# Performance work log

Hardware: AMD Instinct MI355X
Metric: run time of the kernel (lower is better)

The kernel has to match this reference:

```python
import jax, jax.numpy as jnp
import numpy as np

N_NODES = 100000
N_EDGES = 3200000
D = 256
REPEAT = 2
FACTOR = 0.5


def setup_inputs() -> dict:
    key = jax.random.key(0)
    k1, k2, k3, k4, k5, k6 = jax.random.split(key, 6)
    x = jax.random.normal(k1, (N_NODES, D), dtype=jnp.float32)
    vals = jax.random.uniform(k2, (N_EDGES,), dtype=jnp.float32)
    # Xavier-ish scale for linear weights
    W0 = jax.random.normal(k3, (D, D), dtype=jnp.float32) / np.sqrt(D)
    W1 = jax.random.normal(k4, (D, D), dtype=jnp.float32) / np.sqrt(D)
    rows = jax.random.randint(k5, (N_EDGES,), 0, N_NODES, dtype=jnp.int32)
    cols = jax.random.randint(k6, (N_EDGES,), 0, N_NODES, dtype=jnp.int32)
    return {"x": x, "vals": vals, "W0": W0, "W1": W1, "rows": rows, "cols": cols}


def reference(x, vals, W0, W1, rows, cols):
    # support is sparse [N, N] in COO: support[rows[e], cols[e]] = vals[e]
    def spmm(h):
        # gather source-node features, scale by edge weight, scatter-add to dst
        return jax.ops.segment_sum(vals[:, None] * h[cols], rows,
                                   num_segments=N_NODES)

    h = x
    for W, act in ((W0, jax.nn.relu), (W1, lambda v: v)):
        # _propagate: repeated SpMM with scalar factor
        for _ in range(REPEAT):
            h = spmm(h) * FACTOR
        # linear (no bias) + activation
        h = act(h @ W)
    return h
```

## Files before the change

### kernel.cpp

```cpp
#include <hip/hip_runtime.h>
#include <hip/hip_bf16.h>
#include <hip/hip_fp16.h>

#define N_D 256
#define NBLK 832
#define CPB 104
#define RPG_MAX 12512

typedef __attribute__((ext_vector_type(8))) short bf16x8;
typedef __attribute__((ext_vector_type(4))) float f32x4;

__device__ __forceinline__ unsigned short f2bf(float f) {
  union { float f; unsigned u; } c; c.f = f;
  unsigned u = c.u;
  return (unsigned short)((u + 0x7fffu + ((u >> 16) & 1u)) >> 16);
}
__device__ __forceinline__ float asf(unsigned u) {
  union { unsigned u; float f; } c; c.u = u;
  return c.f;
}
__device__ __forceinline__ int grp_of(int r, unsigned gmagic) {
  int g = (int)(((unsigned long long)(unsigned)r * gmagic) >> 37);
  return min(g, 7);
}

template <bool AF32>
__device__ __forceinline__ void gemm_core(
    const void* __restrict__ H, const unsigned short* __restrict__ WT,
    unsigned short* __restrict__ C, int M, int bid) {
  const int wave = threadIdx.x >> 6;
  const int lane = threadIdx.x & 63;
  const int m = lane & 15;
  const int p = lane >> 4;
  const int row0 = bid * 128 + wave * 32;

  f32x4 acc0[16], acc1[16];
#pragma unroll
  for (int i = 0; i < 16; ++i) {
    acc0[i] = (f32x4){0.f, 0.f, 0.f, 0.f};
    acc1[i] = (f32x4){0.f, 0.f, 0.f, 0.f};
  }

  const int r0 = row0 + m;
  const int r1 = row0 + 16 + m;
  const bool ok0 = r0 < M, ok1 = r1 < M;

  for (int k0 = 0; k0 < N_D; k0 += 32) {
    bf16x8 a0 = {0,0,0,0,0,0,0,0}, a1 = {0,0,0,0,0,0,0,0};
    if (AF32) {
      if (ok0) {
        const float* ap = (const float*)H + (size_t)r0 * N_D + k0 + p * 8;
        const float4 f0 = *reinterpret_cast<const float4*>(ap);
        const float4 f1 = *reinterpret_cast<const float4*>(ap + 4);
        a0[0]=f2bf(f0.x); a0[1]=f2bf(f0.y); a0[2]=f2bf(f0.z); a0[3]=f2bf(f0.w);
        a0[4]=f2bf(f1.x); a0[5]=f2bf(f1.y); a0[6]=f2bf(f1.z); a0[7]=f2bf(f1.w);
      }
      if (ok1) {
        const float* ap = (const float*)H + (size_t)r1 * N_D + k0 + p * 8;
        const float4 f0 = *reinterpret_cast<const float4*>(ap);
        const float4 f1 = *reinterpret_cast<const float4*>(ap + 4);
        a1[0]=f2bf(f0.x); a1[1]=f2bf(f0.y); a1[2]=f2bf(f0.z); a1[3]=f2bf(f0.w);
        a1[4]=f2bf(f1.x); a1[5]=f2bf(f1.y); a1[6]=f2bf(f1.z); a1[7]=f2bf(f1.w);
      }
    } else {
      if (ok0) a0 = *reinterpret_cast<const bf16x8*>(
          (const unsigned short*)H + (size_t)r0 * N_D + k0 + p * 8);
      if (ok1) a1 = *reinterpret_cast<const bf16x8*>(
          (const unsigned short*)H + (size_t)r1 * N_D + k0 + p * 8);
    }
#pragma unroll
    for (int nt = 0; nt < 16; ++nt) {
      const bf16x8 b = *reinterpret_cast<const bf16x8*>(
          WT + (size_t)(nt * 16 + m) * N_D + k0 + p * 8);
      acc0[nt] = __builtin_amdgcn_mfma_f32_16x16x32_bf16(a0, b, acc0[nt], 0, 0, 0);
      acc1[nt] = __builtin_amdgcn_mfma_f32_16x16x32_bf16(a1, b, acc1[nt], 0, 0, 0);
    }
  }

#pragma unroll
  for (int nt = 0; nt < 16; ++nt) {
    const int col = nt * 16 + m;
#pragma unroll
    for (int rr = 0; rr < 4; ++rr) {
      const int ra = row0 + p * 4 + rr;
      const int rb = ra + 16;
      if (ra < M) C[(size_t)ra * N_D + col] = f2bf(acc0[nt][rr]);
      if (rb < M) C[(size_t)rb * N_D + col] = f2bf(acc1[nt][rr]);
    }
  }
}

__global__ __launch_bounds__(256) void gemm3_f32(
    const float* __restrict__ H, const unsigned short* __restrict__ WT,
    unsigned short* __restrict__ C, int M) {
  gemm_core<true>(H, WT, C, M, blockIdx.x);
}
__global__ __launch_bounds__(256) void gemm3_bf16(
    const unsigned short* __restrict__ H, const unsigned short* __restrict__ WT,
    unsigned short* __restrict__ C, int M) {
  gemm_core<false>(H, WT, C, M, blockIdx.x);
}

__global__ __launch_bounds__(256) void p0_kernel(
    const int* __restrict__ rows, int* __restrict__ cntT,
    int n_edges, unsigned gmagic,
    const float* __restrict__ W0, const float* __restrict__ W1,
    unsigned short* __restrict__ WT0, unsigned short* __restrict__ WT1) {
  if (blockIdx.x >= NBLK) {
    const int b = blockIdx.x - NBLK;
    const int w = b >> 8;
    const int k = b & 255;
    const int n = threadIdx.x;
    const float* W = w ? W1 : W0;
    unsigned short* WT = w ? WT1 : WT0;
    WT[(size_t)n * N_D + k] = f2bf(W[(size_t)k * N_D + n]);
    return;
  }
  __shared__ int l8[8];
  if (threadIdx.x < 8) l8[threadIdx.x] = 0;
  __syncthreads();
  for (int e = blockIdx.x * 256 + threadIdx.x; e < n_edges; e += NBLK * 256) {
    atomicAdd(&l8[grp_of(rows[e], gmagic)], 1);
  }
  __syncthreads();
  if (threadIdx.x < 8) cntT[threadIdx.x * NBLK + blockIdx.x] = l8[threadIdx.x];
}

__global__ __launch_bounds__(256) void scan_one(
    const int* __restrict__ in, int* __restrict__ out, int n) {
  __shared__ int swsum[4];
  __shared__ int carry_sh;
  const int tid = threadIdx.x;
  const int lane = tid & 63;
  const int wid = tid >> 6;
  if (tid == 0) carry_sh = 0;
  __syncthreads();
  for (int base = 0; base < n; base += 1024) {
    const int i0 = base + tid * 4;
    int4 v = make_int4(0, 0, 0, 0);
    if (i0 + 3 < n) v = *reinterpret_cast<const int4*>(in + i0);
    else {
      if (i0     < n) v.x = in[i0];
      if (i0 + 1 < n) v.y = in[i0 + 1];
      if (i0 + 2 < n) v.z = in[i0 + 2];
    }
    const int s1 = v.x, s2 = s1 + v.y, s3 = s2 + v.z, s4 = s3 + v.w;
    int ws = s4;
#pragma unroll
    for (int off = 1; off < 64; off <<= 1) {
      int o = __shfl_up(ws, off, 64);
      if (lane >= off) ws += o;
    }
    if (lane == 63) swsum[wid] = ws;
    __syncthreads();
    if (wid == 0) {
      int t = (lane < 4) ? swsum[lane] : 0;
#pragma unroll
      for (int off = 1; off < 4; off <<= 1) {
        int o = __shfl_up(t, off, 64);
        if (lane >= off) t += o;
      }
      if (lane < 4) swsum[lane] = t;
    }
    __syncthreads();
    const int carry = carry_sh;
    const int tbase = carry + (wid ? swsum[wid - 1] : 0) + ws - s4;
    if (i0     < n) out[i0]     = tbase;
    if (i0 + 1 < n) out[i0 + 1] = tbase + s1;
    if (i0 + 2 < n) out[i0 + 2] = tbase + s2;
    if (i0 + 3 < n) out[i0 + 3] = tbase + s3;
    __syncthreads();
    if (tid == 0) carry_sh = carry + swsum[3];
    __syncthreads();
  }
  if (tid == 0) out[n] = carry_sh;
}

__global__ __launch_bounds__(256) void partition_kernel(
    const int* __restrict__ rows, const int* __restrict__ cols,
    const float* __restrict__ vals, const int* __restrict__ pofsT,
    int2* __restrict__ part, int n_edges, unsigned gmagic) {
  __shared__ int lofs[8];
  if (threadIdx.x < 8) lofs[threadIdx.x] = pofsT[threadIdx.x * NBLK + blockIdx.x];
  __syncthreads();
  for (int e = blockIdx.x * 256 + threadIdx.x; e < n_edges; e += NBLK * 256) {
    const int r = rows[e];
    const int g = grp_of(r, gmagic);
    const int slot = atomicAdd(&lofs[g], 1);
    const unsigned short hb = __half_as_ushort(__float2half_rn(vals[e] * 0.5f));
    int2 rv;
    rv.x = r;
    rv.y = (int)(((unsigned)cols[e] << 15) | ((unsigned)hb >> 1));
    part[slot] = rv;
  }
}

__global__ __launch_bounds__(256) void hist_kernel(
    const int2* __restrict__ part, const int* __restrict__ pofsT,
    int* __restrict__ cntc, int M, int rpg) {
  const int g = blockIdx.x & 7;
  const int b = blockIdx.x >> 3;
  const int r0 = g * rpg;
  const int nr = min(rpg, M - r0);
  __shared__ int lh[RPG_MAX];
  for (int r = threadIdx.x; r < nr; r += 256) lh[r] = 0;
  __syncthreads();
  const int s0 = pofsT[g * NBLK + b * CPB];
  const int s1 = pofsT[g * NBLK + (b + 1) * CPB];
  for (int i = s0 + threadIdx.x; i < s1; i += 256) {
    atomicAdd(&lh[part[i].x - r0], 1);
  }
  __syncthreads();
  int* dst = cntc + (size_t)(g * 8 + b) * rpg;
  for (int r = threadIdx.x; r < nr; r += 256) dst[r] = lh[r];
}

__global__ __launch_bounds__(256) void sumcnt2_kernel(
    int* __restrict__ cntc, int* __restrict__ cnts,
    int* __restrict__ bsum, int M, int rpg) {
  __shared__ int wred[4];
  const int i = blockIdx.x * 256 + threadIdx.x;
  int s = 0;
  if (i < M) {
    const int g = i / rpg;
    const int rr = i - g * rpg;
    int* base = cntc + (size_t)g * 8 * rpg + rr;
#pragma unroll
    for (int b = 0; b < 8; ++b) {
      const int c = base[(size_t)b * rpg];
      base[(size_t)b * rpg] = s;
      s += c;
    }
    cnts[i] = s;
  }
  int t = s;
#pragma unroll
  for (int off = 32; off; off >>= 1) t += __shfl_down(t, off, 64);
  if ((threadIdx.x & 63) == 0) wred[threadIdx.x >> 6] = t;
  __syncthreads();
  if (threadIdx.x == 0) bsum[blockIdx.x] = wred[0] + wred[1] + wred[2] + wred[3];
}

__global__ __launch_bounds__(256) void apply_kernel(
    const int* __restrict__ cnts, const int* __restrict__ bofs,
    int* __restrict__ row_ptr, int M) {
  __shared__ int wsum[4];
  const int tid = threadIdx.x;
  const int lane = tid & 63;
  const int wid = tid >> 6;
  const int i = blockIdx.x * 256 + tid;
  const int v = (i < M) ? cnts[i] : 0;
  int s = v;
#pragma unroll
  for (int off = 1; off < 64; off <<= 1) {
    int o = __shfl_up(s, off, 64);
    if (lane >= off) s += o;
  }
  if (lane == 63) wsum[wid] = s;
  __syncthreads();
  int add = 0;
  for (int k = 0; k < wid; ++k) add += wsum[k];
  const int excl = bofs[blockIdx.x] + add + s - v;
  if (i < M) row_ptr[i] = excl;
  if (i == M) row_ptr[M] = bofs[gridDim.x];
}

__global__ __launch_bounds__(256) void scatter3_kernel(
    const int2* __restrict__ part, const int* __restrict__ pofsT,
    const int* __restrict__ row_ptr, const int* __restrict__ cntc,
    unsigned* __restrict__ colpack, int M, int rpg) {
  const int g = blockIdx.x & 7;
  const int b = blockIdx.x >> 3;
  const int r0 = g * rpg;
  const int nr = min(rpg, M - r0);
  __shared__ int lc[RPG_MAX];
  const int* pfx = cntc + (size_t)(g * 8 + b) * rpg;
  for (int r = threadIdx.x; r < nr; r += 256)
    lc[r] = row_ptr[r0 + r] + pfx[r];
  __syncthreads();
  const int s0 = pofsT[g * NBLK + b * CPB];
  const int s1 = pofsT[g * NBLK + (b + 1) * CPB];
  for (int i = s0 + threadIdx.x; i < s1; i += 256) {
    const int2 rv = part[i];
    const int pos = atomicAdd(&lc[rv.x - r0], 1);
    colpack[pos] = (unsigned)rv.y;
  }
}

template <bool RELU, bool F32OUT>
__global__ __launch_bounds__(256) void spmm_slice(
    const unsigned short* __restrict__ hin, const int* __restrict__ row_ptr,
    const unsigned* __restrict__ colpack, void* __restrict__ hout,
    int n_nodes) {
  const int slice = blockIdx.x & 3;
  const int lane = threadIdx.x & 63;
  const int half = lane >> 5;
  const int sub  = lane & 31;
  const int wgid = ((blockIdx.x >> 2) * 256 + threadIdx.x) >> 6;
  const int node = wgid * 2 + half;
  const bool ok = node < n_nodes;
  int start = 0, end = 0;
  if (ok) { start = row_ptr[node]; end = row_ptr[node + 1]; }

  const unsigned* __restrict__ hinw = reinterpret_cast<const unsigned*>(hin);
  const int fofs = slice * 32 + sub;
  const int sbase = half << 5;

  float acc0 = 0.f, acc1 = 0.f;

  for (int base = start; base < end; base += 32) {
    const int cnt = min(32, end - base);
    unsigned u = 0;
    if (base + sub < end) u = __builtin_nontemporal_load(&colpack[base + sub]);
    for (int t = 0; t < cnt; t += 8) {
      unsigned hv[8];
      float v[8];
#pragma unroll
      for (int j = 0; j < 8; ++j) {
        const unsigned ue = (unsigned)__shfl((int)u, sbase + t + j, 64);
        const int c = (int)(ue >> 15);
        v[j] = __half2float(__ushort_as_half((unsigned short)(ue << 1)));
        hv[j] = hinw[(size_t)c * 128 + fofs];
      }
#pragma unroll
      for (int j = 0; j < 8; ++j) {
        acc0 += v[j] * asf(hv[j] << 16);
        acc1 += v[j] * asf(hv[j] & 0xffff0000u);
      }
    }
  }
  if (ok) {
    if (RELU) { acc0 = fmaxf(acc0, 0.f); acc1 = fmaxf(acc1, 0.f); }
    if (F32OUT) {
      reinterpret_cast<float2*>(hout)[(size_t)node * 128 + fofs] =
          make_float2(acc0, acc1);
    } else {
      reinterpret_cast<unsigned*>(hout)[(size_t)node * 128 + fofs] =
          (unsigned)f2bf(acc0) | ((unsigned)f2bf(acc1) << 16);
    }
  }
}

extern "C" void kernel_launch(void* const* d_in, const int* in_sizes, int n_in,
                              void* d_out, int out_size, void* d_ws, size_t ws_size,
                              hipStream_t stream) {
  const float* x    = (const float*)d_in[0];
  const float* vals = (const float*)d_in[1];
  const float* W0   = (const float*)d_in[2];
  const float* W1   = (const float*)d_in[3];
  const int*   rows = (const int*)d_in[4];
  const int*   cols = (const int*)d_in[5];

  const int n_edges = in_sizes[1];
  const int M = in_sizes[0] / N_D;
  const size_t n_feat = (size_t)M * N_D;

  char* ws = (char*)d_ws;
  unsigned short* hA      = (unsigned short*)(ws);
  unsigned*       colpack = (unsigned*)(ws + 51200000);
  int*            row_ptr = (int*)(ws + 64000000);
  int*            cnts    = (int*)(ws + 64400128);
  int*            cntc    = (int*)(ws + 64800256);
  int*            bsum    = (int*)(ws + 68000384);
  int*            bofs    = (int*)(ws + 68002944);
  int*            cntT    = (int*)(ws + 68005504);
  int*            pofsT   = (int*)(ws + 68033536);
  unsigned short* wt0     = (unsigned short*)(ws + 68061568);
  unsigned short* wt1     = (unsigned short*)(ws + 68192640);
  unsigned short* hB   = (unsigned short*)d_out;
  unsigned short* hC   = (unsigned short*)d_out + n_feat;
  int2*           part = (int2*)((char*)d_out + 51200000);

  const int Mb = (M + 255) / 256;
  const int sblocks = 4 * ((M + 7) / 8);
  const int gblocks = (M + 127) / 128;
  const int rpg = (M + 7) / 8;
  const unsigned gmagic = (unsigned)(((1ULL << 37) + rpg - 1) / (unsigned long long)rpg);

  p0_kernel<<<NBLK + 512, 256, 0, stream>>>(rows, cntT, n_edges, gmagic,
                                            W0, W1, wt0, wt1);
  scan_one<<<1, 256, 0, stream>>>(cntT, pofsT, 8 * NBLK);
  gemm3_f32<<<gblocks, 256, 0, stream>>>(x, wt0, hB, M);
  partition_kernel<<<NBLK, 256, 0, stream>>>(rows, cols, vals, pofsT, part,
                                             n_edges, gmagic);
  hist_kernel<<<64, 256, 0, stream>>>(part, pofsT, cntc, M, rpg);
  sumcnt2_kernel<<<Mb, 256, 0, stream>>>(cntc, cnts, bsum, M, rpg);
  scan_one<<<1, 256, 0, stream>>>(bsum, bofs, Mb);
  apply_kernel<<<Mb, 256, 0, stream>>>(cnts, bofs, row_ptr, M);
  scatter3_kernel<<<64, 256, 0, stream>>>(part, pofsT, row_ptr, cntc,
                                          colpack, M, rpg);

  spmm_slice<false, false><<<sblocks, 256, 0, stream>>>(hB, row_ptr, colpack, hA, M);
  spmm_slice<true,  false><<<sblocks, 256, 0, stream>>>(hA, row_ptr, colpack, hB, M);

  gemm3_bf16<<<gblocks, 256, 0, stream>>>(hB, wt1, hC, M);
  spmm_slice<false, false><<<sblocks, 256, 0, stream>>>(hC, row_ptr, colpack, hA, M);
  spmm_slice<false, true ><<<sblocks, 256, 0, stream>>>(hA, row_ptr, colpack, d_out, M);
}
```

Baseline: 1.125 ms.

## Fuse first GEMM into partition launch and double hist/scatter chunk count

The first dense GEMM (x@W0) now runs as extra blocks of the partition kernel, so the two independent stages share one launch and can overlap. Hist and scatter now split each row group into 16 chunks instead of 8 (CPB halved), giving 128 blocks instead of 64 for more parallelism in the CSR build. The per-chunk count buffer moves into spare space in the output buffer because it doubled in size. The trade-offs are a longer prefix loop in sumcnt2 and mixed block types in one grid.

```diff
diff --git a/kernel.cpp b/kernel.cpp
--- a/kernel.cpp
+++ b/kernel.cpp
@@ -4,7 +4,8 @@
 
 #define N_D 256
 #define NBLK 832
-#define CPB 104
+#define CPB 52
+#define NCH 16
 #define RPG_MAX 12512
 
 typedef __attribute__((ext_vector_type(8))) short bf16x8;
@@ -90,11 +91,6 @@
   }
 }
 
-__global__ __launch_bounds__(256) void gemm3_f32(
-    const float* __restrict__ H, const unsigned short* __restrict__ WT,
-    unsigned short* __restrict__ C, int M) {
-  gemm_core<true>(H, WT, C, M, blockIdx.x);
-}
 __global__ __launch_bounds__(256) void gemm3_bf16(
     const unsigned short* __restrict__ H, const unsigned short* __restrict__ WT,
     unsigned short* __restrict__ C, int M) {
@@ -176,10 +172,16 @@
   if (tid == 0) out[n] = carry_sh;
 }
 
-__global__ __launch_bounds__(256) void partition_kernel(
+__global__ __launch_bounds__(256) void fatpg_kernel(
     const int* __restrict__ rows, const int* __restrict__ cols,
     const float* __restrict__ vals, const int* __restrict__ pofsT,
-    int2* __restrict__ part, int n_edges, unsigned gmagic) {
+    int2* __restrict__ part, int n_edges, unsigned gmagic,
+    const float* __restrict__ x, const unsigned short* __restrict__ WT0,
+    unsigned short* __restrict__ hB, int M) {
+  if (blockIdx.x >= NBLK) {
+    gemm_core<true>(x, WT0, hB, M, blockIdx.x - NBLK);
+    return;
+  }
   __shared__ int lofs[8];
   if (threadIdx.x < 8) lofs[threadIdx.x] = pofsT[threadIdx.x * NBLK + blockIdx.x];
   __syncthreads();
@@ -211,7 +213,7 @@
     atomicAdd(&lh[part[i].x - r0], 1);
   }
   __syncthreads();
-  int* dst = cntc + (size_t)(g * 8 + b) * rpg;
+  int* dst = cntc + (size_t)(g * NCH + b) * rpg;
   for (int r = threadIdx.x; r < nr; r += 256) dst[r] = lh[r];
 }
 
@@ -224,9 +226,9 @@
   if (i < M) {
     const int g = i / rpg;
     const int rr = i - g * rpg;
-    int* base = cntc + (size_t)g * 8 * rpg + rr;
-#pragma unroll
-    for (int b = 0; b < 8; ++b) {
+    int* base = cntc + (size_t)g * NCH * rpg + rr;
+#pragma unroll
+    for (int b = 0; b < NCH; ++b) {
       const int c = base[(size_t)b * rpg];
       base[(size_t)b * rpg] = s;
       s += c;
@@ -274,7 +276,7 @@
   const int r0 = g * rpg;
   const int nr = min(rpg, M - r0);
   __shared__ int lc[RPG_MAX];
-  const int* pfx = cntc + (size_t)(g * 8 + b) * rpg;
+  const int* pfx = cntc + (size_t)(g * NCH + b) * rpg;
   for (int r = threadIdx.x; r < nr; r += 256)
     lc[r] = row_ptr[r0 + r] + pfx[r];
   __syncthreads();
@@ -360,16 +362,16 @@
   unsigned*       colpack = (unsigned*)(ws + 51200000);
   int*            row_ptr = (int*)(ws + 64000000);
   int*            cnts    = (int*)(ws + 64400128);
-  int*            cntc    = (int*)(ws + 64800256);
-  int*            bsum    = (int*)(ws + 68000384);
-  int*            bofs    = (int*)(ws + 68002944);
-  int*            cntT    = (int*)(ws + 68005504);
-  int*            pofsT   = (int*)(ws + 68033536);
-  unsigned short* wt0     = (unsigned short*)(ws + 68061568);
-  unsigned short* wt1     = (unsigned short*)(ws + 68192640);
+  int*            bsum    = (int*)(ws + 64800256);
+  int*            bofs    = (int*)(ws + 64802816);
+  int*            cntT    = (int*)(ws + 64805376);
+  int*            pofsT   = (int*)(ws + 64832000);
+  unsigned short* wt0     = (unsigned short*)(ws + 64858880);
+  unsigned short* wt1     = (unsigned short*)(ws + 64989952);
   unsigned short* hB   = (unsigned short*)d_out;
   unsigned short* hC   = (unsigned short*)d_out + n_feat;
   int2*           part = (int2*)((char*)d_out + 51200000);
+  int*            cntc = (int*)((char*)d_out + 76800000);
 
   const int Mb = (M + 255) / 256;
   const int sblocks = 4 * ((M + 7) / 8);
@@ -380,15 +382,14 @@
   p0_kernel<<<NBLK + 512, 256, 0, stream>>>(rows, cntT, n_edges, gmagic,
                                             W0, W1, wt0, wt1);
   scan_one<<<1, 256, 0, stream>>>(cntT, pofsT, 8 * NBLK);
-  gemm3_f32<<<gblocks, 256, 0, stream>>>(x, wt0, hB, M);
-  partition_kernel<<<NBLK, 256, 0, stream>>>(rows, cols, vals, pofsT, part,
-                                             n_edges, gmagic);
-  hist_kernel<<<64, 256, 0, stream>>>(part, pofsT, cntc, M, rpg);
+  fatpg_kernel<<<NBLK + gblocks, 256, 0, stream>>>(rows, cols, vals, pofsT, part,
+                                                   n_edges, gmagic, x, wt0, hB, M);
+  hist_kernel<<<8 * NCH, 256, 0, stream>>>(part, pofsT, cntc, M, rpg);
   sumcnt2_kernel<<<Mb, 256, 0, stream>>>(cntc, cnts, bsum, M, rpg);
   scan_one<<<1, 256, 0, stream>>>(bsum, bofs, Mb);
   apply_kernel<<<Mb, 256, 0, stream>>>(cnts, bofs, row_ptr, M);
-  scatter3_kernel<<<64, 256, 0, stream>>>(part, pofsT, row_ptr, cntc,
-                                          colpack, M, rpg);
+  scatter3_kernel<<<8 * NCH, 256, 0, stream>>>(part, pofsT, row_ptr, cntc,
+                                               colpack, M, rpg);
 
   spmm_slice<false, false><<<sblocks, 256, 0, stream>>>(hB, row_ptr, colpack, hA, M);
   spmm_slice<true,  false><<<sblocks, 256, 0, stream>>>(hA, row_ptr, colpack, hB, M);
```

Result: faster. 1.077 ms (-4.3%).
